# Performance work log

Measured on AMD Instinct MI355X. Metric: run time of the kernel, lower is better.

Reference implementation:

```python
import jax, jax.numpy as jnp
import numpy as np

EPS = 1e-5
HEADS, KK, UU, VV, MM = 4, 16, 1, 64, 23
PAD = (MM - 1) // 2


def _bn(x, gamma, beta, mean, var):
    # eval-mode BatchNorm2d over channel axis 1 of (b, c, w, h)
    scale = gamma / jnp.sqrt(var + EPS)
    return (x - mean[:, None, None]) * scale[:, None, None] + beta[:, None, None]


def setup_inputs() -> dict:
    key = jax.random.key(0)
    ks = jax.random.split(key, 13)
    B, C, W, H = 8, 256, 64, 64
    return {
        "x": jax.random.normal(ks[0], (B, C, W, H), jnp.float32),
        "Wq": jax.random.normal(ks[1], (KK * HEADS, C), jnp.float32) * 0.05,
        "q_gamma": jax.random.uniform(ks[2], (KK * HEADS,), jnp.float32),
        "q_beta": jax.random.normal(ks[3], (KK * HEADS,), jnp.float32) * 0.05,
        "q_mean": jax.random.normal(ks[4], (KK * HEADS,), jnp.float32) * 0.05,
        "q_var": jax.random.uniform(ks[5], (KK * HEADS,), jnp.float32) + 0.5,
        "Wk": jax.random.normal(ks[6], (KK * UU, C), jnp.float32) * 0.05,
        "Wv": jax.random.normal(ks[7], (VV * UU, C), jnp.float32) * 0.05,
        "v_gamma": jax.random.uniform(ks[8], (VV * UU,), jnp.float32),
        "v_beta": jax.random.normal(ks[9], (VV * UU,), jnp.float32) * 0.05,
        "v_mean": jax.random.normal(ks[10], (VV * UU,), jnp.float32) * 0.05,
        "v_var": jax.random.uniform(ks[11], (VV * UU,), jnp.float32) + 0.5,
        "embedding": jax.random.normal(ks[12], (KK, UU, 1, MM, MM), jnp.float32),
    }


def reference(x, Wq, q_gamma, q_beta, q_mean, q_var, Wk, Wv, v_gamma, v_beta, v_mean, v_var, embedding):
    b, C, w, h = x.shape
    n = w * h
    # 1x1 conv projections as channel GEMMs
    q = jnp.einsum('bcij,oc->boij', x, Wq)
    q = _bn(q, q_gamma, q_beta, q_mean, q_var).reshape(b, HEADS, KK, n)
    kf = jnp.einsum('bcij,oc->boij', x, Wk).reshape(b, KK, UU, n)
    kf = jax.nn.softmax(kf, axis=-1)  # softmax over spatial positions
    v = jnp.einsum('bcij,oc->boij', x, Wv)
    v = _bn(v, v_gamma, v_beta, v_mean, v_var)  # (b, vv*uu, w, h)
    v_flat = v.reshape(b, VV, UU, n)
    # content lambda
    lambda_c = jnp.einsum('bkum,bvum->bkv', kf, v_flat)
    y_c = jnp.einsum('bhkn,bkv->bhvn', q, lambda_c)
    # positional lambda via depth-1 conv3d over (vv, w, h)
    v5 = v.reshape(b, UU, VV, w, h)
    lambda_p = jax.lax.conv_general_dilated(
        v5, embedding, window_strides=(1, 1, 1),
        padding=[(0, 0), (PAD, PAD), (PAD, PAD)],
        dimension_numbers=('NCDHW', 'OIDHW', 'NCDHW'))  # (b, kk, vv, w, h)
    lambda_p = lambda_p.reshape(b, KK, VV, n)
    y_p = jnp.einsum('bhkn,bkvn->bhvn', q, lambda_p)
    out = (y_c + y_p).reshape(b, HEADS * VV, w, h)
    return out
```

## Files before the change

kernel.cpp:

```cpp
#include <hip/hip_runtime.h>

typedef __attribute__((ext_vector_type(8))) short bf16x8;
typedef __attribute__((ext_vector_type(4))) float f32x4;

#define EPS 1e-5f
#define B 8
#define C 256
#define NPIX 4096
#define NCH 144
#define ROW_V 64
#define ROW_KF 128
#define PAD 11
#define VH_WORDS 3840

#define WP_OFF    0u
#define BIAS_OFF  36864u
#define PROJ_OFF  37120u
#define RMAX_OFF  4755712u
#define RSC_OFF   4755840u
#define LC_OFF    4755968u
#define ET_OFF    4764160u
#define QT_OFF    4811264u
#define OUTT_OFF  6908416u
#define WS_NEED_QT    6908416u
#define WS_NEED_FULL  15297024u

__device__ inline short f2bf(float f) {
  unsigned u = __float_as_uint(f);
  return (short)((u + 0x7fffu + ((u >> 16) & 1u)) >> 16);
}

__global__ __launch_bounds__(256) void k_wfold(
    const float* __restrict__ Wq, const float* __restrict__ qg, const float* __restrict__ qb,
    const float* __restrict__ qm, const float* __restrict__ qv,
    const float* __restrict__ Wk, const float* __restrict__ Wv,
    const float* __restrict__ vg, const float* __restrict__ vb,
    const float* __restrict__ vm, const float* __restrict__ vvar,
    float* __restrict__ Wt, float* __restrict__ biasp) {
  int o = blockIdx.x;
  int t = threadIdx.x;
  const float* src; float s, bias;
  if (o < 64) {
    s = qg[o] * rsqrtf(qv[o] + EPS); bias = qb[o] - qm[o] * s; src = Wq + o * C;
  } else if (o < 128) {
    int i = o - 64;
    s = vg[i] * rsqrtf(vvar[i] + EPS); bias = vb[i] - vm[i] * s; src = Wv + i * C;
  } else {
    int i = o - 128; s = 1.f; bias = 0.f; src = Wk + i * C;
  }
  Wt[t * NCH + o] = src[t] * s;
  if (t == 0) biasp[o] = bias;
}

__global__ __launch_bounds__(256) void k_eprep(
    const float* __restrict__ emb, ushort* __restrict__ etw) {
  int i = blockIdx.x * 256 + threadIdx.x;
  int s = i / 11776;
  int r = i % 11776;
  int dy = r / 512;
  int l = (r / 8) % 64;
  int jj = r % 8;
  int f = l & 15, q = l >> 4;
  int dx = q * 8 + jj - s;
  float val = (dx >= 0 && dx < 23) ? emb[f * 529 + dy * 23 + dx] : 0.f;
  unsigned u = __float_as_uint(val);
  etw[i] = (ushort)((u + 0x7fffu + ((u >> 16) & 1u)) >> 16);
}

__global__ __launch_bounds__(256) void k_proj(
    const float* __restrict__ x, const float* __restrict__ Wt,
    const float* __restrict__ biasp, float* __restrict__ proj) {
  int tile = blockIdx.x;
  int g = blockIdx.y;
  int b = blockIdx.z;
  int t = threadIdx.x;
  int px = tile * 256 + t;
  const float* xb = x + (size_t)b * C * NPIX + px;
  float acc[18];
  #pragma unroll
  for (int i = 0; i < 18; i++) acc[i] = 0.f;
  #pragma unroll 4
  for (int c = 0; c < C; c++) {
    float xv = xb[(size_t)c * NPIX];
    const float* wrow = Wt + c * NCH + g * 18;
    #pragma unroll
    for (int i = 0; i < 18; i++) acc[i] += xv * wrow[i];
  }
  float* ob = proj + ((size_t)b * NCH + g * 18) * NPIX + px;
  #pragma unroll
  for (int i = 0; i < 18; i++) ob[(size_t)i * NPIX] = acc[i] + biasp[g * 18 + i];
}

__global__ __launch_bounds__(256) void k_qtrans(
    const float* __restrict__ proj, float* __restrict__ qT) {
  int ch = blockIdx.x, b = blockIdx.y, t = threadIdx.x;
  __shared__ float buf[4608];
  const float* src = proj + ((size_t)b * NCH + ch) * NPIX;
  for (int it = 0; it < 16; it++) {
    int p = it * 256 + t;
    buf[p + (p >> 3)] = src[p];
  }
  __syncthreads();
  float* dst = qT + ((size_t)b * 64 + ch) * NPIX;
  for (int it = 0; it < 16; it++) {
    int idx = it * 256 + t;
    int s = idx >> 9, i = idx & 511;
    int p = (i >> 3) * 64 + (i & 7) * 8 + s;
    dst[idx] = buf[p + (p >> 3)];
  }
}

__global__ __launch_bounds__(256) void k_vhalo(
    const float* __restrict__ proj, uint* __restrict__ vhg) {
  int v = blockIdx.x, b = blockIdx.y, t = threadIdx.x;
  const float* vrow = proj + ((size_t)b * NCH + ROW_V + v) * NPIX;
  uint* dst = vhg + (size_t)b * NCH * NPIX + (size_t)v * VH_WORDS;
  for (int p2 = t; p2 < 3784; p2 += 256) {
    int hr = p2 / 44;
    int hc = (p2 % 44) * 2;
    int ir = hr - 11;
    int ic0 = hc - 11, ic1 = hc - 10;
    bool rok = (ir >= 0 && ir < 64);
    float f0 = (rok && ic0 >= 0 && ic0 < 64) ? vrow[ir * 64 + ic0] : 0.f;
    float f1 = (rok && ic1 >= 0 && ic1 < 64) ? vrow[ir * 64 + ic1] : 0.f;
    uint u0 = __float_as_uint(f0), u1 = __float_as_uint(f1);
    uint h0 = (u0 + 0x7fffu + ((u0 >> 16) & 1u)) >> 16;
    uint h1 = (u1 + 0x7fffu + ((u1 >> 16) & 1u)) >> 16;
    dst[p2] = (h0 & 0xffffu) | (h1 << 16);
  }
}

__global__ __launch_bounds__(256) void k_softstat(
    const float* __restrict__ proj, float* __restrict__ rmax, float* __restrict__ rsc) {
  int k = blockIdx.x, b = blockIdx.y, t = threadIdx.x;
  const float* row = proj + ((size_t)b * NCH + ROW_KF + k) * NPIX;
  __shared__ float sd[256];
  float m = -1e30f;
  for (int n = t; n < NPIX; n += 256) m = fmaxf(m, row[n]);
  sd[t] = m; __syncthreads();
  for (int s = 128; s > 0; s >>= 1) { if (t < s) sd[t] = fmaxf(sd[t], sd[t + s]); __syncthreads(); }
  m = sd[0]; __syncthreads();
  float sum = 0.f;
  for (int n = t; n < NPIX; n += 256) sum += __expf(row[n] - m);
  sd[t] = sum; __syncthreads();
  for (int s = 128; s > 0; s >>= 1) { if (t < s) sd[t] += sd[t + s]; __syncthreads(); }
  if (t == 0) { rmax[b * 16 + k] = m; rsc[b * 16 + k] = 1.f / sd[0]; }
}

__global__ __launch_bounds__(256) void k_lambda_c(
    const float* __restrict__ proj, const float* __restrict__ rmax,
    const float* __restrict__ rsc, float* __restrict__ lc) {
  int split = blockIdx.x;
  int b = blockIdx.y;
  int t = threadIdx.x;
  int lane = t & 63, w = t >> 6;
  int kr = lane & 15;
  int half = lane >> 4;
  float m = rmax[b * 16 + kr], sc = rsc[b * 16 + kr];
  const float* kfrow = proj + ((size_t)b * NCH + ROW_KF + kr) * NPIX;
  const float* vrow  = proj + ((size_t)b * NCH + ROW_V + w * 16 + kr) * NPIX;
  f32x4 acc = (f32x4)(0.f);
  #pragma unroll
  for (int c = 0; c < 2; c++) {
    int n0 = split * 64 + c * 32 + half * 8;
    float4 fa0 = *(const float4*)(kfrow + n0);
    float4 fa1 = *(const float4*)(kfrow + n0 + 4);
    float4 fb0 = *(const float4*)(vrow + n0);
    float4 fb1 = *(const float4*)(vrow + n0 + 4);
    bf16x8 a, bb;
    a[0] = f2bf(__expf(fa0.x - m) * sc); a[1] = f2bf(__expf(fa0.y - m) * sc);
    a[2] = f2bf(__expf(fa0.z - m) * sc); a[3] = f2bf(__expf(fa0.w - m) * sc);
    a[4] = f2bf(__expf(fa1.x - m) * sc); a[5] = f2bf(__expf(fa1.y - m) * sc);
    a[6] = f2bf(__expf(fa1.z - m) * sc); a[7] = f2bf(__expf(fa1.w - m) * sc);
    bb[0] = f2bf(fb0.x); bb[1] = f2bf(fb0.y); bb[2] = f2bf(fb0.z); bb[3] = f2bf(fb0.w);
    bb[4] = f2bf(fb1.x); bb[5] = f2bf(fb1.y); bb[6] = f2bf(fb1.z); bb[7] = f2bf(fb1.w);
    acc = __builtin_amdgcn_mfma_f32_16x16x32_bf16(a, bb, acc, 0, 0, 0);
  }
  #pragma unroll
  for (int r = 0; r < 4; r++) {
    int k = half * 4 + r;
    atomicAdd(&lc[((size_t)b * 16 + k) * 64 + w * 16 + kr], acc[r]);
  }
}

__global__ __launch_bounds__(256, 2) void k_conv_mfma(
    const float* __restrict__ proj, const ushort* __restrict__ etw,
    const float* __restrict__ qT, const float* __restrict__ lc,
    const uint* __restrict__ vhg,
    float* __restrict__ outT, float* __restrict__ out, int mode) {
  int s = blockIdx.x;
  int v = blockIdx.y;
  int b = blockIdx.z;
  int t = threadIdx.x;
  __shared__ __align__(16) ushort vh[86 * 88];
  __shared__ __align__(16) ushort elds[23 * 64 * 8];

  {
    const uint4* src = (const uint4*)etw + s * 1472;
    uint4* dst = (uint4*)elds;
    for (int i = t; i < 1472; i += 256) dst[i] = src[i];
  }
  if (mode != 0) {
    const uint4* vsrc = (const uint4*)(vhg + (size_t)b * NCH * NPIX + (size_t)v * VH_WORDS);
    uint4* vdst = (uint4*)vh;
    for (int i = t; i < 946; i += 256) vdst[i] = vsrc[i];
  } else {
    const float* vrow = proj + ((size_t)b * NCH + ROW_V + v) * NPIX;
    for (int i = t; i < 86 * 88; i += 256) {
      int hr = i / 88, hc = i % 88;
      int ir = hr - 11, ic = hc - 11;
      float val = (ir >= 0 && ir < 64 && ic >= 0 && ic < 64) ? vrow[ir * 64 + ic] : 0.f;
      unsigned u = __float_as_uint(val);
      vh[i] = (ushort)((u + 0x7fffu + ((u >> 16) & 1u)) >> 16);
    }
  }
  __syncthreads();

  int lane = t & 63, w = t >> 6;
  int n_ = lane & 15, q = lane >> 4;
  int rn = n_ >> 3, g = n_ & 7;

  f32x4 acc[8];
  #pragma unroll
  for (int i = 0; i < 8; i++) acc[i] = (f32x4)(0.f);

  const bf16x8* vh8 = (const bf16x8*)vh;
  const bf16x8* e8 = (const bf16x8*)elds;
  int baseA = (w * 16 + rn) * 11 + g + q;

  bf16x8 bfr[16];
  #pragma unroll
  for (int r = 0; r < 16; r++)
    bfr[(r & 1) * 8 + ((r >> 1) & 7)] = vh8[baseA + r * 11];

  #pragma unroll
  for (int dy = 0; dy < 23; dy++) {
    bf16x8 ef = e8[dy * 64 + lane];
    bf16x8 tmp;
    if (dy + 16 <= 36) tmp = vh8[baseA + (dy + 16) * 11];
    #pragma unroll
    for (int tt = 0; tt < 8; tt++) {
      int r = dy + 2 * tt;
      acc[tt] = __builtin_amdgcn_mfma_f32_16x16x32_bf16(
          ef, bfr[(r & 1) * 8 + ((r >> 1) & 7)], acc[tt], 0, 0, 0);
    }
    if (dy + 16 <= 36) {
      int rr = dy + 16;
      bfr[(rr & 1) * 8 + ((rr >> 1) & 7)] = tmp;
    }
  }

  float lcv[4];
  #pragma unroll
  for (int r = 0; r < 4; r++) lcv[r] = lc[((size_t)b * 16 + q * 4 + r) * 64 + v];

  if (mode != 0) {
    const float* qTb = qT + (size_t)b * 64 * NPIX;
    float* obT = outT + (size_t)b * 256 * NPIX;
    float* ob = out + (size_t)b * 256 * NPIX;
    #pragma unroll
    for (int tt = 0; tt < 8; tt++) {
      int row = w * 16 + 2 * tt + rn;
      int io = s * 512 + row * 8 + g;
      float lam[4];
      #pragma unroll
      for (int r = 0; r < 4; r++) lam[r] = acc[tt][r] + lcv[r];
      float y[4];
      #pragma unroll
      for (int h = 0; h < 4; h++) {
        float a = 0.f;
        #pragma unroll
        for (int r = 0; r < 4; r++)
          a += qTb[(size_t)(h * 16 + q * 4 + r) * NPIX + io] * lam[r];
        y[h] = a;
      }
      #pragma unroll
      for (int h = 0; h < 4; h++) {
        y[h] += __shfl_xor(y[h], 16);
        y[h] += __shfl_xor(y[h], 32);
      }
      if (q == 0) {
        if (mode == 2) {
          #pragma unroll
          for (int h = 0; h < 4; h++) obT[(size_t)(h * 64 + v) * NPIX + io] = y[h];
        } else {
          int p = row * 64 + 8 * g + s;
          #pragma unroll
          for (int h = 0; h < 4; h++) ob[(size_t)(h * 64 + v) * NPIX + p] = y[h];
        }
      }
    }
  } else {
    const float* qbp = proj + (size_t)b * NCH * NPIX;
    float* ob = out + (size_t)b * 256 * NPIX;
    #pragma unroll
    for (int tt = 0; tt < 8; tt++) {
      int p = (w * 16 + 2 * tt + rn) * 64 + 8 * g + s;
      float lam[4];
      #pragma unroll
      for (int r = 0; r < 4; r++) lam[r] = acc[tt][r] + lcv[r];
      float y[4];
      #pragma unroll
      for (int h = 0; h < 4; h++) {
        float a = 0.f;
        #pragma unroll
        for (int r = 0; r < 4; r++)
          a += qbp[(size_t)(h * 16 + q * 4 + r) * NPIX + p] * lam[r];
        y[h] = a;
      }
      #pragma unroll
      for (int h = 0; h < 4; h++) {
        y[h] += __shfl_xor(y[h], 16);
        y[h] += __shfl_xor(y[h], 32);
      }
      if (q == 0) {
        #pragma unroll
        for (int h = 0; h < 4; h++) ob[(size_t)(h * 64 + v) * NPIX + p] = y[h];
      }
    }
  }
}

__global__ __launch_bounds__(256) void k_outtrans(
    const float* __restrict__ outT, float* __restrict__ out) {
  int ch = blockIdx.x, b = blockIdx.y, t = threadIdx.x;
  __shared__ float buf[4608];
  const float* src = outT + ((size_t)b * 256 + ch) * NPIX;
  for (int it = 0; it < 16; it++) {
    int idx = it * 256 + t;
    int s = idx >> 9, i = idx & 511;
    int p = (i >> 3) * 64 + (i & 7) * 8 + s;
    buf[p + (p >> 3)] = src[idx];
  }
  __syncthreads();
  float* dst = out + ((size_t)b * 256 + ch) * NPIX;
  for (int it = 0; it < 16; it++) {
    int p = it * 256 + t;
    dst[p] = buf[p + (p >> 3)];
  }
}

extern "C" void kernel_launch(void* const* d_in, const int* in_sizes, int n_in,
                              void* d_out, int out_size, void* d_ws, size_t ws_size,
                              hipStream_t stream) {
  const float* x    = (const float*)d_in[0];
  const float* Wq   = (const float*)d_in[1];
  const float* qg   = (const float*)d_in[2];
  const float* qbta = (const float*)d_in[3];
  const float* qm   = (const float*)d_in[4];
  const float* qv   = (const float*)d_in[5];
  const float* Wk   = (const float*)d_in[6];
  const float* Wv   = (const float*)d_in[7];
  const float* vg   = (const float*)d_in[8];
  const float* vb   = (const float*)d_in[9];
  const float* vm   = (const float*)d_in[10];
  const float* vvar = (const float*)d_in[11];
  const float* emb  = (const float*)d_in[12];
  float* ws   = (float*)d_ws;
  float* Wt   = ws + WP_OFF;
  float* bp   = ws + BIAS_OFF;
  float* proj = ws + PROJ_OFF;
  float* rmax = ws + RMAX_OFF;
  float* rsc  = ws + RSC_OFF;
  float* lcw  = ws + LC_OFF;
  ushort* etw = (ushort*)(ws + ET_OFF);
  float* qT   = ws + QT_OFF;
  float* outT = ws + OUTT_OFF;
  float* out  = (float*)d_out;
  uint* vhg   = (uint*)proj;

  size_t wsf = ws_size / sizeof(float);
  int mode = (wsf >= WS_NEED_FULL) ? 2 : ((wsf >= WS_NEED_QT) ? 1 : 0);

  hipLaunchKernelGGL(k_wfold, dim3(144), dim3(256), 0, stream,
                     Wq, qg, qbta, qm, qv, Wk, Wv, vg, vb, vm, vvar, Wt, bp);
  hipLaunchKernelGGL(k_eprep, dim3(368), dim3(256), 0, stream, emb, etw);
  hipMemsetAsync(lcw, 0, 16 * 64 * B * sizeof(float), stream);
  hipLaunchKernelGGL(k_proj, dim3(16, 8, 8), dim3(256), 0, stream, x, Wt, bp, proj);
  if (mode >= 1) {
    hipLaunchKernelGGL(k_qtrans, dim3(64, 8), dim3(256), 0, stream, proj, qT);
    hipLaunchKernelGGL(k_vhalo, dim3(64, 8), dim3(256), 0, stream, proj, vhg);
  }
  hipLaunchKernelGGL(k_softstat, dim3(16, 8), dim3(256), 0, stream, proj, rmax, rsc);
  hipLaunchKernelGGL(k_lambda_c, dim3(64, 8), dim3(256), 0, stream, proj, rmax, rsc, lcw);
  hipLaunchKernelGGL(k_conv_mfma, dim3(8, 64, 8), dim3(256), 0, stream,
                     proj, etw, qT, lcw, vhg, outT, out, mode);
  if (mode == 2)
    hipLaunchKernelGGL(k_outtrans, dim3(256, 8), dim3(256), 0, stream, outT, out);
}
```

Before: 234.7 us.

## Compute 1x1 projection GEMM with bf16 MFMA instead of scalar FP32 loop

```diff
diff --git a/kernel.cpp b/kernel.cpp
--- a/kernel.cpp
+++ b/kernel.cpp
@@ -52,6 +52,24 @@
   if (t == 0) biasp[o] = bias;
 }
 
+__global__ __launch_bounds__(256) void k_wprep(
+    const float* __restrict__ Wt, ushort* __restrict__ wtA) {
+  int i = blockIdx.x * 256 + threadIdx.x;
+  int mt = i >> 9;
+  int rest = i & 511;
+  int kt = rest >> 6;
+  int lane = rest & 63;
+  int m = mt * 16 + (lane & 15);
+  int c0 = kt * 32 + (lane >> 4) * 8;
+  ushort* dst = wtA + (size_t)i * 8;
+  #pragma unroll
+  for (int j = 0; j < 8; j++) {
+    float v = Wt[(c0 + j) * NCH + m];
+    unsigned u = __float_as_uint(v);
+    dst[j] = (ushort)((u + 0x7fffu + ((u >> 16) & 1u)) >> 16);
+  }
+}
+
 __global__ __launch_bounds__(256) void k_eprep(
     const float* __restrict__ emb, ushort* __restrict__ etw) {
   int i = blockIdx.x * 256 + threadIdx.x;
@@ -65,6 +83,43 @@
   float val = (dx >= 0 && dx < 23) ? emb[f * 529 + dy * 23 + dx] : 0.f;
   unsigned u = __float_as_uint(val);
   etw[i] = (ushort)((u + 0x7fffu + ((u >> 16) & 1u)) >> 16);
+}
+
+__global__ __launch_bounds__(256) void k_projm(
+    const float* __restrict__ x, const ushort* __restrict__ wtA,
+    const float* __restrict__ biasp, float* __restrict__ proj) {
+  int ntile = blockIdx.x;
+  int b = blockIdx.y;
+  int t = threadIdx.x;
+  int lane = t & 63, w = t >> 6;
+  int px = ntile * 64 + w * 16 + (lane & 15);
+  int kq = lane >> 4;
+  const float* xb = x + (size_t)b * C * NPIX + px;
+  const bf16x8* A = (const bf16x8*)wtA;
+  f32x4 acc[9];
+  #pragma unroll
+  for (int i = 0; i < 9; i++) acc[i] = (f32x4)(0.f);
+  #pragma unroll 2
+  for (int kt = 0; kt < 8; kt++) {
+    int c0 = kt * 32 + kq * 8;
+    bf16x8 bb;
+    #pragma unroll
+    for (int j = 0; j < 8; j++) bb[j] = f2bf(xb[(size_t)(c0 + j) * NPIX]);
+    #pragma unroll
+    for (int mt = 0; mt < 9; mt++) {
+      bf16x8 a = A[(mt * 8 + kt) * 64 + lane];
+      acc[mt] = __builtin_amdgcn_mfma_f32_16x16x32_bf16(a, bb, acc[mt], 0, 0, 0);
+    }
+  }
+  float* pb = proj + (size_t)b * NCH * NPIX + px;
+  #pragma unroll
+  for (int mt = 0; mt < 9; mt++) {
+    #pragma unroll
+    for (int r = 0; r < 4; r++) {
+      int ch = mt * 16 + kq * 4 + r;
+      pb[(size_t)ch * NPIX] = acc[mt][r] + biasp[ch];
+    }
+  }
 }
 
 __global__ __launch_bounds__(256) void k_proj(
@@ -368,6 +423,7 @@
   float* outT = ws + OUTT_OFF;
   float* out  = (float*)d_out;
   uint* vhg   = (uint*)proj;
+  ushort* wtA = (ushort*)qT;
 
   size_t wsf = ws_size / sizeof(float);
   int mode = (wsf >= WS_NEED_FULL) ? 2 : ((wsf >= WS_NEED_QT) ? 1 : 0);
@@ -376,10 +432,13 @@
                      Wq, qg, qbta, qm, qv, Wk, Wv, vg, vb, vm, vvar, Wt, bp);
   hipLaunchKernelGGL(k_eprep, dim3(368), dim3(256), 0, stream, emb, etw);
   hipMemsetAsync(lcw, 0, 16 * 64 * B * sizeof(float), stream);
-  hipLaunchKernelGGL(k_proj, dim3(16, 8, 8), dim3(256), 0, stream, x, Wt, bp, proj);
   if (mode >= 1) {
+    hipLaunchKernelGGL(k_wprep, dim3(18), dim3(256), 0, stream, Wt, wtA);
+    hipLaunchKernelGGL(k_projm, dim3(64, 8), dim3(256), 0, stream, x, wtA, bp, proj);
     hipLaunchKernelGGL(k_qtrans, dim3(64, 8), dim3(256), 0, stream, proj, qT);
     hipLaunchKernelGGL(k_vhalo, dim3(64, 8), dim3(256), 0, stream, proj, vhg);
+  } else {
+    hipLaunchKernelGGL(k_proj, dim3(16, 8, 8), dim3(256), 0, stream, x, Wt, bp, proj);
   }
   hipLaunchKernelGGL(k_softstat, dim3(16, 8), dim3(256), 0, stream, proj, rmax, rsc);
   hipLaunchKernelGGL(k_lambda_c, dim3(64, 8), dim3(256), 0, stream, proj, rmax, rsc, lcw);
```

Result: faster. 217.1 us (-7.5%).
